# Performance work log

Hardware: AMD Instinct MI355X
Metric: run time of the kernel (lower is better)

Reference implementation:

```python
import jax, jax.numpy as jnp
import numpy as np

UNITS = 1024
OUT_STEPS = 32
NUM_FEATURES = 4
BATCH = 1024
IN_STEPS = 64


def setup_inputs() -> dict:
    key = jax.random.key(0)
    k = jax.random.split(key, 6)
    x = jax.random.normal(k[0], (BATCH, IN_STEPS, NUM_FEATURES), jnp.float32)
    # Keras LSTMCell params: kernel [F,4u], recurrent_kernel [u,4u], bias [4u]
    W = jax.random.normal(k[1], (NUM_FEATURES, 4 * UNITS), jnp.float32) * 0.3
    U = jax.random.normal(k[2], (UNITS, 4 * UNITS), jnp.float32) * 0.03
    b = jnp.zeros((4 * UNITS,), jnp.float32)
    Wd = jax.random.normal(k[3], (UNITS, NUM_FEATURES), jnp.float32) * 0.05
    bd = jnp.zeros((NUM_FEATURES,), jnp.float32)
    return {"x": x, "W": W, "U": U, "b": b, "Wd": Wd, "bd": bd}


def _lstm_cell(xt, h, c, W, U, b):
    # Keras gate order: input, forget, cell, output; sigmoid recurrent act, tanh act
    z = xt @ W + h @ U + b  # [B, 4u]
    i, f, g, o = jnp.split(z, 4, axis=-1)
    c_new = jax.nn.sigmoid(f) * c + jax.nn.sigmoid(i) * jnp.tanh(g)
    h_new = jax.nn.sigmoid(o) * jnp.tanh(c_new)
    return h_new, c_new


def reference(x, W, U, b, Wd, bd):
    B = x.shape[0]
    h0 = jnp.zeros((B, UNITS), x.dtype)
    c0 = jnp.zeros((B, UNITS), x.dtype)

    # warmup: run RNN over the input window, keep final state
    def warm_step(carry, xt):
        h, c = carry
        h, c = _lstm_cell(xt, h, c, W, U, b)
        return (h, c), None

    (h, c), _ = jax.lax.scan(warm_step, (h0, c0), jnp.swapaxes(x, 0, 1))
    pred0 = h @ Wd + bd  # first prediction [B, F]

    def dec_step(carry, _):
        pred, h, c = carry
        h, c = _lstm_cell(pred, h, c, W, U, b)
        pred = h @ Wd + bd
        return (pred, h, c), pred

    _, preds = jax.lax.scan(dec_step, (pred0, h, c), None, length=OUT_STEPS - 1)
    all_preds = jnp.concatenate([pred0[None], preds], axis=0)  # [out_steps, B, F]
    return jnp.transpose(all_preds, (1, 0, 2))  # [B, out_steps, F]
```

## Files before the change

### kernel.cpp

```cpp
#include <hip/hip_runtime.h>

#define BATCH    1024
#define UNITS    1024
#define INSTEPS  64
#define OUTSTEPS 32
#define NF       4
#define NSTEPS   (INSTEPS + OUTSTEPS - 1)

typedef _Float16 half8 __attribute__((ext_vector_type(8)));
typedef float    f32x4 __attribute__((ext_vector_type(4)));

__device__ __forceinline__ float sigf(float x)  { return 1.0f / (1.0f + __expf(-x)); }
__device__ __forceinline__ float tanhf_(float x){ return 1.0f - 2.0f / (__expf(2.0f * x) + 1.0f); }

__global__ void u_transpose(const float* __restrict__ U, _Float16* __restrict__ Ut) {
    __shared__ _Float16 T[64][72];
    const int tid = threadIdx.x;
    const int bid = blockIdx.x;
    const int k0 = (bid >> 6) << 6;
    const int n0 = (bid & 63) << 6;
    #pragma unroll
    for (int i = 0; i < 16; ++i) {
        int q = i * 256 + tid;
        int r = q >> 6, cc = q & 63;
        T[r][cc] = (_Float16)U[(size_t)(k0 + r) * 4096 + n0 + cc];
    }
    __syncthreads();
    #pragma unroll
    for (int i = 0; i < 16; ++i) {
        int q = i * 256 + tid;
        int nn = q >> 6, kk = q & 63;
        Ut[(size_t)(n0 + nn) * 1024 + k0 + kk] = T[kk][nn];
    }
}

#define BS_BYTES  (16*64*64*2)
#define XS_BYTES  (256*4*4)
#define HST_OFF   (BS_BYTES + XS_BYTES)
#define HST_BYTES (256*18*2)
#define LDS_BYTES (HST_OFF + HST_BYTES)

__global__ __launch_bounds__(512, 2) void lstm_seq(
    const float* __restrict__ x, const float* __restrict__ W,
    const float* __restrict__ bias, const float* __restrict__ Wd,
    const float* __restrict__ bd, const _Float16* __restrict__ Ut,
    _Float16* hA, _Float16* hB, float* out, unsigned* bar)
{
    extern __shared__ __align__(16) char smem[];
    _Float16 (*Bs)[64][64] = (_Float16 (*)[64][64])smem;
    float (*xs)[NF] = (float (*)[NF])(smem + BS_BYTES);
    _Float16 (*hst)[18] = (_Float16 (*)[18])(smem + HST_OFF);

    const int tid  = threadIdx.x;
    const int bid  = blockIdx.x;
    const int band = bid & 3;
    const int m0   = band << 8;
    const int u0   = (bid >> 2) << 4;

    const int lane = tid & 63;
    const int wv   = tid >> 6;
    const int quad = lane >> 4;
    const int ln   = lane & 15;

    unsigned* cnt = bar + band * 64;

    const int r_st = tid >> 3;
    const int ck   = tid & 7;
    const int swz  = ((ck ^ (r_st & 7)) << 3);
    const int n_st = ((r_st >> 4) << 10) + u0 + (r_st & 15);
    const _Float16* bsrc = Ut + (size_t)n_st * UNITS + ck * 8;

    #pragma unroll
    for (int kc = 0; kc < 16; ++kc)
        *(float4*)&Bs[kc][r_st][swz] = *(const float4*)(bsrc + kc * 64);

    float wt[4][4], bt[4], btp[4];
    #pragma unroll
    for (int g = 0; g < 4; ++g) {
        int col = (g << 10) + u0 + ln;
        bt[g] = bias[col];
        #pragma unroll
        for (int f = 0; f < 4; ++f) wt[g][f] = W[f * 4096 + col];
    }
    {
        float bdr0 = bd[0], bdr1 = bd[1], bdr2 = bd[2], bdr3 = bd[3];
        #pragma unroll
        for (int g = 0; g < 4; ++g)
            btp[g] = bt[g] + bdr0*wt[g][0] + bdr1*wt[g][1] + bdr2*wt[g][2] + bdr3*wt[g][3];
    }
    const float* wdp = Wd + (size_t)(u0 + ln) * NF;
    float wd0 = wdp[0], wd1 = wdp[1], wd2 = wdp[2], wd3 = wdp[3];
    float bd0 = 0, bd1 = 0, bd2 = 0, bd3 = 0;
    if (u0 == 0) { bd0 = bd[0]; bd1 = bd[1]; bd2 = bd[2]; bd3 = bd[3]; }

    float cr[2][4] = {{0,0,0,0},{0,0,0,0}};
    float hnv[2][4];

    const int swz0 = ((quad ^ (ln & 7)) << 3);
    const int swz1 = swz0 ^ 32;

    const int row0 = m0 + wv * 32 + ln;
    const int aoff = ((quad >> 1) << 15) + row0 * 32 + ((quad & 1) << 4);

    const int xr = tid >> 2, xf = tid & 3;
    float xp0 = x[(size_t)(m0 + xr) * (INSTEPS * NF) + xf];
    float xp1 = x[(size_t)(m0 + 128 + xr) * (INSTEPS * NF) + xf];

    char* const hAc = (char*)hA;
    char* const hBc = (char*)hB;
    const size_t stoff = ((size_t)(u0 >> 4) << 15) + (size_t)(m0 + (tid >> 1)) * 32
                       + ((size_t)(tid & 1) << 4);

    __syncthreads();

    for (int p = 0; p < NSTEPS; ++p) {
        if (p < INSTEPS) {
            xs[xr][xf]       = xp0;
            xs[128 + xr][xf] = xp1;
        } else if (p == INSTEPS) {
            float wc0 = W[n_st], wc1 = W[4096 + n_st],
                  wc2 = W[8192 + n_st], wc3 = W[12288 + n_st];
            #pragma unroll
            for (int kc = 0; kc < 16; ++kc) {
                int k0 = kc * 64 + ck * 8;
                half8 uv = *(const half8*)(bsrc + kc * 64);
                half8 tv;
                #pragma unroll
                for (int j = 0; j < 8; ++j) {
                    const float* wdr = Wd + (size_t)(k0 + j) * NF;
                    float corr = wdr[0]*wc0 + wdr[1]*wc1 + wdr[2]*wc2 + wdr[3]*wc3;
                    tv[j] = (_Float16)((float)uv[j] + corr);
                }
                *(half8*)&Bs[kc][r_st][swz] = tv;
            }
        }
        if (p <= INSTEPS) __syncthreads();

        f32x4 acc[2][4] = {};

        if (p > 0) {
            const char* hb = ((p & 1) ? hAc : hBc) + aoff;
#define AL(kc, j, rr) (*(const half8*)(hb + ((((kc) << 2) + ((j) << 1)) << 15) + ((rr) << 9)))

            half8 ar[6][4];
            #pragma unroll
            for (int d = 0; d < 6; ++d) {
                ar[d][0] = AL(d, 0, 0);
                ar[d][1] = AL(d, 1, 0);
                ar[d][2] = AL(d, 0, 1);
                ar[d][3] = AL(d, 1, 1);
            }

            #pragma unroll
            for (int kc = 0; kc < 16; ++kc) {
                const int sl = kc % 6;
                half8 af0 = ar[sl][0], ag0 = ar[sl][1], af1 = ar[sl][2], ag1 = ar[sl][3];
                if (kc < 10) {
                    ar[sl][0] = AL(kc + 6, 0, 0);
                    ar[sl][1] = AL(kc + 6, 1, 0);
                    ar[sl][2] = AL(kc + 6, 0, 1);
                    ar[sl][3] = AL(kc + 6, 1, 1);
                }
                const _Float16 (*B)[64] = Bs[kc];
                half8 bf0 = *(const half8*)&B[ln][swz0];
                half8 bf1 = *(const half8*)&B[16 + ln][swz0];
                half8 bf2 = *(const half8*)&B[32 + ln][swz0];
                half8 bf3 = *(const half8*)&B[48 + ln][swz0];
                acc[0][0] = __builtin_amdgcn_mfma_f32_16x16x32_f16(af0, bf0, acc[0][0], 0, 0, 0);
                acc[1][0] = __builtin_amdgcn_mfma_f32_16x16x32_f16(af1, bf0, acc[1][0], 0, 0, 0);
                acc[0][1] = __builtin_amdgcn_mfma_f32_16x16x32_f16(af0, bf1, acc[0][1], 0, 0, 0);
                acc[1][1] = __builtin_amdgcn_mfma_f32_16x16x32_f16(af1, bf1, acc[1][1], 0, 0, 0);
                acc[0][2] = __builtin_amdgcn_mfma_f32_16x16x32_f16(af0, bf2, acc[0][2], 0, 0, 0);
                acc[1][2] = __builtin_amdgcn_mfma_f32_16x16x32_f16(af1, bf2, acc[1][2], 0, 0, 0);
                acc[0][3] = __builtin_amdgcn_mfma_f32_16x16x32_f16(af0, bf3, acc[0][3], 0, 0, 0);
                acc[1][3] = __builtin_amdgcn_mfma_f32_16x16x32_f16(af1, bf3, acc[1][3], 0, 0, 0);
                half8 bg0 = *(const half8*)&B[ln][swz1];
                half8 bg1 = *(const half8*)&B[16 + ln][swz1];
                half8 bg2 = *(const half8*)&B[32 + ln][swz1];
                half8 bg3 = *(const half8*)&B[48 + ln][swz1];
                acc[0][0] = __builtin_amdgcn_mfma_f32_16x16x32_f16(ag0, bg0, acc[0][0], 0, 0, 0);
                acc[1][0] = __builtin_amdgcn_mfma_f32_16x16x32_f16(ag1, bg0, acc[1][0], 0, 0, 0);
                acc[0][1] = __builtin_amdgcn_mfma_f32_16x16x32_f16(ag0, bg1, acc[0][1], 0, 0, 0);
                acc[1][1] = __builtin_amdgcn_mfma_f32_16x16x32_f16(ag1, bg1, acc[1][1], 0, 0, 0);
                acc[0][2] = __builtin_amdgcn_mfma_f32_16x16x32_f16(ag0, bg2, acc[0][2], 0, 0, 0);
                acc[1][2] = __builtin_amdgcn_mfma_f32_16x16x32_f16(ag1, bg2, acc[1][2], 0, 0, 0);
                acc[0][3] = __builtin_amdgcn_mfma_f32_16x16x32_f16(ag0, bg3, acc[0][3], 0, 0, 0);
                acc[1][3] = __builtin_amdgcn_mfma_f32_16x16x32_f16(ag1, bg3, acc[1][3], 0, 0, 0);
            }
#undef AL
        }

        const int s_out = p - (INSTEPS - 1);
        #pragma unroll
        for (int r = 0; r < 2; ++r) {
            #pragma unroll
            for (int i = 0; i < 4; ++i) {
                int rl = wv * 32 + r * 16 + quad * 4 + i;
                float zi, zf, zg, zo;
                if (p < INSTEPS) {
                    float x0 = xs[rl][0], x1 = xs[rl][1], x2 = xs[rl][2], x3 = xs[rl][3];
                    zi = acc[r][0][i] + bt[0] + x0*wt[0][0] + x1*wt[0][1] + x2*wt[0][2] + x3*wt[0][3];
                    zf = acc[r][1][i] + bt[1] + x0*wt[1][0] + x1*wt[1][1] + x2*wt[1][2] + x3*wt[1][3];
                    zg = acc[r][2][i] + bt[2] + x0*wt[2][0] + x1*wt[2][1] + x2*wt[2][2] + x3*wt[2][3];
                    zo = acc[r][3][i] + bt[3] + x0*wt[3][0] + x1*wt[3][1] + x2*wt[3][2] + x3*wt[3][3];
                } else {
                    zi = acc[r][0][i] + btp[0];
                    zf = acc[r][1][i] + btp[1];
                    zg = acc[r][2][i] + btp[2];
                    zo = acc[r][3][i] + btp[3];
                }
                float cold = cr[r][i];
                float si = sigf(zi), sf = sigf(zf), so = sigf(zo);
                float cn = sf * cold + si * tanhf_(zg);
                float hn = so * tanhf_(cn);
                cr[r][i] = cn;
                hnv[r][i] = hn;
                hst[rl][ln] = (_Float16)hn;
            }
        }

        const int pn = p + 1;

        {
            char* hw = (p & 1) ? hBc : hAc;
            const unsigned long long* sp = (const unsigned long long*)
                ((const char*)hst + (tid >> 1) * 36 + ((tid & 1) << 4));
            unsigned long long v0 = sp[0], v1 = sp[1];
            unsigned long long* dst = (unsigned long long*)(hw + stoff);
            __hip_atomic_store(dst,     v0, __ATOMIC_RELAXED, __HIP_MEMORY_SCOPE_AGENT);
            __hip_atomic_store(dst + 1, v1, __ATOMIC_RELAXED, __HIP_MEMORY_SCOPE_AGENT);
        }

        __syncthreads();
        if (tid == 0)
            __hip_atomic_fetch_add(cnt, 1u, __ATOMIC_RELAXED, __HIP_MEMORY_SCOPE_AGENT);

        if (s_out >= 0) {
            #pragma unroll
            for (int r = 0; r < 2; ++r) {
                #pragma unroll
                for (int i = 0; i < 4; ++i) {
                    float hn = hnv[r][i];
                    float p0 = hn * wd0, p1 = hn * wd1, p2 = hn * wd2, p3 = hn * wd3;
                    #pragma unroll
                    for (int mk = 1; mk < 16; mk <<= 1) {
                        p0 += __shfl_xor(p0, mk);
                        p1 += __shfl_xor(p1, mk);
                        p2 += __shfl_xor(p2, mk);
                        p3 += __shfl_xor(p3, mk);
                    }
                    if (ln == 0) {
                        int R = m0 + wv * 32 + r * 16 + quad * 4 + i;
                        float* op = out + (size_t)R * (OUTSTEPS * NF) + s_out * NF;
                        atomicAdd(op + 0, p0 + bd0);
                        atomicAdd(op + 1, p1 + bd1);
                        atomicAdd(op + 2, p2 + bd2);
                        atomicAdd(op + 3, p3 + bd3);
                    }
                }
            }
        }

        if (pn < INSTEPS) {
            xp0 = x[(size_t)(m0 + xr) * (INSTEPS * NF) + pn * NF + xf];
            xp1 = x[(size_t)(m0 + 128 + xr) * (INSTEPS * NF) + pn * NF + xf];
        }

        if (tid == 0) {
            const unsigned tgt = (unsigned)pn * 64u;
            while (__hip_atomic_load(cnt, __ATOMIC_RELAXED, __HIP_MEMORY_SCOPE_AGENT) < tgt)
                __builtin_amdgcn_s_sleep(1);
            __builtin_amdgcn_fence(__ATOMIC_ACQUIRE, "agent");
        }
        __syncthreads();
    }
}

extern "C" void kernel_launch(void* const* d_in, const int* in_sizes, int n_in,
                              void* d_out, int out_size, void* d_ws, size_t ws_size,
                              hipStream_t stream) {
    (void)in_sizes; (void)n_in; (void)ws_size;
    const float* x  = (const float*)d_in[0];
    const float* W  = (const float*)d_in[1];
    const float* U  = (const float*)d_in[2];
    const float* b  = (const float*)d_in[3];
    const float* Wd = (const float*)d_in[4];
    const float* bd = (const float*)d_in[5];
    float* out = (float*)d_out;

    char* ws = (char*)d_ws;
    _Float16* hA  = (_Float16*)ws;
    _Float16* hB  = (_Float16*)(ws + (2 << 20));
    _Float16* Ut  = (_Float16*)(ws + (4 << 20));
    unsigned* bar = (unsigned*)(ws + (12 << 20));

    hipMemsetAsync(bar, 0, 4096, stream);
    hipMemsetAsync(d_out, 0, (size_t)out_size * sizeof(float), stream);
    u_transpose<<<1024, 256, 0, stream>>>(U, Ut);

    hipFuncSetAttribute((const void*)lstm_seq,
                        hipFuncAttributeMaxDynamicSharedMemorySize, LDS_BYTES);

    void* args[] = {(void*)&x, (void*)&W, (void*)&b, (void*)&Wd, (void*)&bd,
                    (void*)&Ut, (void*)&hA, (void*)&hB, (void*)&out, (void*)&bar};
    hipLaunchCooperativeKernel((const void*)lstm_seq, dim3(256), dim3(512),
                               args, LDS_BYTES, stream);
}
```

Before: 1.952 ms.

## Replace per-band grid barrier with per-K-chunk group flags consumed inside GEMM

Each band's single counter and full spin barrier at the end of every step are replaced by 16 per-group counters, one per group of 16 blocks. Each counter covers the hidden-state slice that feeds one K-chunk. Before loading a K-chunk of h, a wave waits only on the flag for that chunk's producers and reads h with relaxed agent-scope atomic loads. This lets the recurrent GEMM start on chunks that are already ready, overlapping with blocks that are still finishing. The trade-off is more flag polling per wave, split 8-byte atomic loads in place of 16-byte vector loads, and no acquire fence, which relies on relaxed atomics for visibility. The removed trailing __syncthreads may also leave LDS reuse across steps less protected.

After: 3.453 ms. 1.77x slower.

```diff
diff --git a/kernel.cpp b/kernel.cpp
--- a/kernel.cpp
+++ b/kernel.cpp
@@ -62,7 +62,8 @@
     const int quad = lane >> 4;
     const int ln   = lane & 15;
 
-    unsigned* cnt = bar + band * 64;
+    unsigned* flg = bar + band * 16;
+    const int mygrp = bid >> 4;
 
     const int r_st = tid >> 3;
     const int ck   = tid & 7;
@@ -140,15 +141,42 @@
 
         if (p > 0) {
             const char* hb = ((p & 1) ? hAc : hBc) + aoff;
-#define AL(kc, j, rr) (*(const half8*)(hb + ((((kc) << 2) + ((j) << 1)) << 15) + ((rr) << 9)))
+            const unsigned need = 4u * (unsigned)p;
+
+            unsigned fv = 0xFFFFFFFFu;
+            if (lane < 16)
+                fv = __hip_atomic_load(&flg[lane], __ATOMIC_RELAXED, __HIP_MEMORY_SCOPE_AGENT);
+            unsigned long long rdy = __ballot(fv >= need);
+
+#define WAITG(g) do {                                                           \
+        if (!((rdy >> (g)) & 1)) {                                              \
+            while (__hip_atomic_load(&flg[(g)], __ATOMIC_RELAXED,               \
+                                     __HIP_MEMORY_SCOPE_AGENT) < need)          \
+                __builtin_amdgcn_s_sleep(1);                                    \
+        }                                                                       \
+        asm volatile("" ::: "memory");                                          \
+    } while (0)
+
+#define AL8(dst, off) do {                                                      \
+        unsigned long long _a = __hip_atomic_load(                              \
+            (const unsigned long long*)(hb + (off)),                            \
+            __ATOMIC_RELAXED, __HIP_MEMORY_SCOPE_AGENT);                        \
+        unsigned long long _b = __hip_atomic_load(                              \
+            (const unsigned long long*)(hb + (off) + 8),                        \
+            __ATOMIC_RELAXED, __HIP_MEMORY_SCOPE_AGENT);                        \
+        union { unsigned long long u[2]; half8 h; } _v;                         \
+        _v.u[0] = _a; _v.u[1] = _b; (dst) = _v.h;                               \
+    } while (0)
+#define AOFF(kc, j, rr) (((((kc) << 2) + ((j) << 1)) << 15) + ((rr) << 9))
 
             half8 ar[6][4];
             #pragma unroll
             for (int d = 0; d < 6; ++d) {
-                ar[d][0] = AL(d, 0, 0);
-                ar[d][1] = AL(d, 1, 0);
-                ar[d][2] = AL(d, 0, 1);
-                ar[d][3] = AL(d, 1, 1);
+                WAITG(d);
+                AL8(ar[d][0], AOFF(d, 0, 0));
+                AL8(ar[d][1], AOFF(d, 1, 0));
+                AL8(ar[d][2], AOFF(d, 0, 1));
+                AL8(ar[d][3], AOFF(d, 1, 1));
             }
 
             #pragma unroll
@@ -156,10 +184,11 @@
                 const int sl = kc % 6;
                 half8 af0 = ar[sl][0], ag0 = ar[sl][1], af1 = ar[sl][2], ag1 = ar[sl][3];
                 if (kc < 10) {
-                    ar[sl][0] = AL(kc + 6, 0, 0);
-                    ar[sl][1] = AL(kc + 6, 1, 0);
-                    ar[sl][2] = AL(kc + 6, 0, 1);
-                    ar[sl][3] = AL(kc + 6, 1, 1);
+                    WAITG(kc + 6);
+                    AL8(ar[sl][0], AOFF(kc + 6, 0, 0));
+                    AL8(ar[sl][1], AOFF(kc + 6, 1, 0));
+                    AL8(ar[sl][2], AOFF(kc + 6, 0, 1));
+                    AL8(ar[sl][3], AOFF(kc + 6, 1, 1));
                 }
                 const _Float16 (*B)[64] = Bs[kc];
                 half8 bf0 = *(const half8*)&B[ln][swz0];
@@ -187,7 +216,9 @@
                 acc[0][3] = __builtin_amdgcn_mfma_f32_16x16x32_f16(ag0, bg3, acc[0][3], 0, 0, 0);
                 acc[1][3] = __builtin_amdgcn_mfma_f32_16x16x32_f16(ag1, bg3, acc[1][3], 0, 0, 0);
             }
-#undef AL
+#undef AOFF
+#undef AL8
+#undef WAITG
         }
 
         const int s_out = p - (INSTEPS - 1);
@@ -219,8 +250,6 @@
             }
         }
 
-        const int pn = p + 1;
-
         {
             char* hw = (p & 1) ? hBc : hAc;
             const unsigned long long* sp = (const unsigned long long*)
@@ -233,7 +262,7 @@
 
         __syncthreads();
         if (tid == 0)
-            __hip_atomic_fetch_add(cnt, 1u, __ATOMIC_RELAXED, __HIP_MEMORY_SCOPE_AGENT);
+            __hip_atomic_fetch_add(&flg[mygrp], 1u, __ATOMIC_RELAXED, __HIP_MEMORY_SCOPE_AGENT);
 
         if (s_out >= 0) {
             #pragma unroll
@@ -261,18 +290,11 @@
             }
         }
 
+        const int pn = p + 1;
         if (pn < INSTEPS) {
             xp0 = x[(size_t)(m0 + xr) * (INSTEPS * NF) + pn * NF + xf];
             xp1 = x[(size_t)(m0 + 128 + xr) * (INSTEPS * NF) + pn * NF + xf];
         }
-
-        if (tid == 0) {
-            const unsigned tgt = (unsigned)pn * 64u;
-            while (__hip_atomic_load(cnt, __ATOMIC_RELAXED, __HIP_MEMORY_SCOPE_AGENT) < tgt)
-                __builtin_amdgcn_s_sleep(1);
-            __builtin_amdgcn_fence(__ATOMIC_ACQUIRE, "agent");
-        }
-        __syncthreads();
     }
 }
 
```

## Split K across two wave halves per block with LDS reduction

Applied to the files above, without the earlier changes.

Doubles the block size to 1024 threads and splits the recurrent GEMM's K dimension in half. Each group of 8 waves computes partial sums over 8 k-chunks, and the two halves are combined through an LDS exchange buffer over four rounds of barriers. Only the first half then runs the gate math, the h store and the dense projection. The aim is to shorten the per-step critical path, more waves hiding global h-load latency. The cost is extra LDS traffic, eight more __syncthreads per step, and idle upper waves during the elementwise phase.

After: 1.847 ms. 1.06x faster.

```diff
diff --git a/kernel.cpp b/kernel.cpp
--- a/kernel.cpp
+++ b/kernel.cpp
@@ -38,9 +38,11 @@
 #define XS_BYTES  (256*4*4)
 #define HST_OFF   (BS_BYTES + XS_BYTES)
 #define HST_BYTES (256*18*2)
-#define LDS_BYTES (HST_OFF + HST_BYTES)
-
-__global__ __launch_bounds__(512, 2) void lstm_seq(
+#define XB_OFF    (HST_OFF + HST_BYTES)
+#define XB_BYTES  (2*8*64*16)
+#define LDS_BYTES (XB_OFF + XB_BYTES)
+
+__global__ __launch_bounds__(1024, 4) void lstm_seq(
     const float* __restrict__ x, const float* __restrict__ W,
     const float* __restrict__ bias, const float* __restrict__ Wd,
     const float* __restrict__ bd, const _Float16* __restrict__ Ut,
@@ -50,6 +52,7 @@
     _Float16 (*Bs)[64][64] = (_Float16 (*)[64][64])smem;
     float (*xs)[NF] = (float (*)[NF])(smem + BS_BYTES);
     _Float16 (*hst)[18] = (_Float16 (*)[18])(smem + HST_OFF);
+    f32x4 (*xb)[8][64] = (f32x4 (*)[8][64])(smem + XB_OFF);
 
     const int tid  = threadIdx.x;
     const int bid  = blockIdx.x;
@@ -59,20 +62,24 @@
 
     const int lane = tid & 63;
     const int wv   = tid >> 6;
+    const int rt2  = wv & 7;
+    const int kh   = wv >> 3;
     const int quad = lane >> 4;
     const int ln   = lane & 15;
 
     unsigned* cnt = bar + band * 64;
 
-    const int r_st = tid >> 3;
+    const int r_st = (tid >> 3) & 63;
     const int ck   = tid & 7;
     const int swz  = ((ck ^ (r_st & 7)) << 3);
     const int n_st = ((r_st >> 4) << 10) + u0 + (r_st & 15);
     const _Float16* bsrc = Ut + (size_t)n_st * UNITS + ck * 8;
 
-    #pragma unroll
-    for (int kc = 0; kc < 16; ++kc)
-        *(float4*)&Bs[kc][r_st][swz] = *(const float4*)(bsrc + kc * 64);
+    if (tid < 512) {
+        #pragma unroll
+        for (int kc = 0; kc < 16; ++kc)
+            *(float4*)&Bs[kc][r_st][swz] = *(const float4*)(bsrc + kc * 64);
+    }
 
     float wt[4][4], bt[4], btp[4];
     #pragma unroll
@@ -99,12 +106,11 @@
     const int swz0 = ((quad ^ (ln & 7)) << 3);
     const int swz1 = swz0 ^ 32;
 
-    const int row0 = m0 + wv * 32 + ln;
+    const int row0 = m0 + rt2 * 32 + ln;
     const int aoff = ((quad >> 1) << 15) + row0 * 32 + ((quad & 1) << 4);
 
     const int xr = tid >> 2, xf = tid & 3;
     float xp0 = x[(size_t)(m0 + xr) * (INSTEPS * NF) + xf];
-    float xp1 = x[(size_t)(m0 + 128 + xr) * (INSTEPS * NF) + xf];
 
     char* const hAc = (char*)hA;
     char* const hBc = (char*)hB;
@@ -115,9 +121,8 @@
 
     for (int p = 0; p < NSTEPS; ++p) {
         if (p < INSTEPS) {
-            xs[xr][xf]       = xp0;
-            xs[128 + xr][xf] = xp1;
-        } else if (p == INSTEPS) {
+            xs[xr][xf] = xp0;
+        } else if (p == INSTEPS && tid < 512) {
             float wc0 = W[n_st], wc1 = W[4096 + n_st],
                   wc2 = W[8192 + n_st], wc3 = W[12288 + n_st];
             #pragma unroll
@@ -140,28 +145,30 @@
 
         if (p > 0) {
             const char* hb = ((p & 1) ? hAc : hBc) + aoff;
-#define AL(kc, j, rr) (*(const half8*)(hb + ((((kc) << 2) + ((j) << 1)) << 15) + ((rr) << 9)))
-
-            half8 ar[6][4];
-            #pragma unroll
-            for (int d = 0; d < 6; ++d) {
-                ar[d][0] = AL(d, 0, 0);
-                ar[d][1] = AL(d, 1, 0);
-                ar[d][2] = AL(d, 0, 1);
-                ar[d][3] = AL(d, 1, 1);
-            }
-
-            #pragma unroll
-            for (int kc = 0; kc < 16; ++kc) {
-                const int sl = kc % 6;
+#define AL(kcg, j, rr) (*(const half8*)(hb + ((((kcg) << 2) + ((j) << 1)) << 15) + ((rr) << 9)))
+
+            half8 ar[2][4];
+            #pragma unroll
+            for (int d = 0; d < 2; ++d) {
+                const int kcg = (kh << 3) + d;
+                ar[d][0] = AL(kcg, 0, 0);
+                ar[d][1] = AL(kcg, 1, 0);
+                ar[d][2] = AL(kcg, 0, 1);
+                ar[d][3] = AL(kcg, 1, 1);
+            }
+
+            #pragma unroll
+            for (int kc = 0; kc < 8; ++kc) {
+                const int sl = kc & 1;
                 half8 af0 = ar[sl][0], ag0 = ar[sl][1], af1 = ar[sl][2], ag1 = ar[sl][3];
-                if (kc < 10) {
-                    ar[sl][0] = AL(kc + 6, 0, 0);
-                    ar[sl][1] = AL(kc + 6, 1, 0);
-                    ar[sl][2] = AL(kc + 6, 0, 1);
-                    ar[sl][3] = AL(kc + 6, 1, 1);
-                }
-                const _Float16 (*B)[64] = Bs[kc];
+                if (kc < 6) {
+                    const int kcg = (kh << 3) + kc + 2;
+                    ar[sl][0] = AL(kcg, 0, 0);
+                    ar[sl][1] = AL(kcg, 1, 0);
+                    ar[sl][2] = AL(kcg, 0, 1);
+                    ar[sl][3] = AL(kcg, 1, 1);
+                }
+                const _Float16 (*B)[64] = Bs[(kh << 3) + kc];
                 half8 bf0 = *(const half8*)&B[ln][swz0];
                 half8 bf1 = *(const half8*)&B[16 + ln][swz0];
                 half8 bf2 = *(const half8*)&B[32 + ln][swz0];
@@ -188,54 +195,73 @@
                 acc[1][3] = __builtin_amdgcn_mfma_f32_16x16x32_f16(ag1, bg3, acc[1][3], 0, 0, 0);
             }
 #undef AL
+
+            #pragma unroll
+            for (int r = 0; r < 4; ++r) {
+                if ((wv >> 1) == 4 + r) {
+                    #pragma unroll
+                    for (int j = 0; j < 8; ++j)
+                        xb[wv & 1][j][lane] = acc[j >> 2][j & 3];
+                }
+                __syncthreads();
+                if ((wv >> 1) == r) {
+                    #pragma unroll
+                    for (int j = 0; j < 8; ++j)
+                        acc[j >> 2][j & 3] += xb[wv & 1][j][lane];
+                }
+                __syncthreads();
+            }
         }
 
         const int s_out = p - (INSTEPS - 1);
-        #pragma unroll
-        for (int r = 0; r < 2; ++r) {
-            #pragma unroll
-            for (int i = 0; i < 4; ++i) {
-                int rl = wv * 32 + r * 16 + quad * 4 + i;
-                float zi, zf, zg, zo;
-                if (p < INSTEPS) {
-                    float x0 = xs[rl][0], x1 = xs[rl][1], x2 = xs[rl][2], x3 = xs[rl][3];
-                    zi = acc[r][0][i] + bt[0] + x0*wt[0][0] + x1*wt[0][1] + x2*wt[0][2] + x3*wt[0][3];
-                    zf = acc[r][1][i] + bt[1] + x0*wt[1][0] + x1*wt[1][1] + x2*wt[1][2] + x3*wt[1][3];
-                    zg = acc[r][2][i] + bt[2] + x0*wt[2][0] + x1*wt[2][1] + x2*wt[2][2] + x3*wt[2][3];
-                    zo = acc[r][3][i] + bt[3] + x0*wt[3][0] + x1*wt[3][1] + x2*wt[3][2] + x3*wt[3][3];
-                } else {
-                    zi = acc[r][0][i] + btp[0];
-                    zf = acc[r][1][i] + btp[1];
-                    zg = acc[r][2][i] + btp[2];
-                    zo = acc[r][3][i] + btp[3];
-                }
-                float cold = cr[r][i];
-                float si = sigf(zi), sf = sigf(zf), so = sigf(zo);
-                float cn = sf * cold + si * tanhf_(zg);
-                float hn = so * tanhf_(cn);
-                cr[r][i] = cn;
-                hnv[r][i] = hn;
-                hst[rl][ln] = (_Float16)hn;
+
+        if (kh == 0) {
+            #pragma unroll
+            for (int r = 0; r < 2; ++r) {
+                #pragma unroll
+                for (int i = 0; i < 4; ++i) {
+                    int rl = rt2 * 32 + r * 16 + quad * 4 + i;
+                    float zi, zf, zg, zo;
+                    if (p < INSTEPS) {
+                        float x0 = xs[rl][0], x1 = xs[rl][1], x2 = xs[rl][2], x3 = xs[rl][3];
+                        zi = acc[r][0][i] + bt[0] + x0*wt[0][0] + x1*wt[0][1] + x2*wt[0][2] + x3*wt[0][3];
+                        zf = acc[r][1][i] + bt[1] + x0*wt[1][0] + x1*wt[1][1] + x2*wt[1][2] + x3*wt[1][3];
+                        zg = acc[r][2][i] + bt[2] + x0*wt[2][0] + x1*wt[2][1] + x2*wt[2][2] + x3*wt[2][3];
+                        zo = acc[r][3][i] + bt[3] + x0*wt[3][0] + x1*wt[3][1] + x2*wt[3][2] + x3*wt[3][3];
+                    } else {
+                        zi = acc[r][0][i] + btp[0];
+                        zf = acc[r][1][i] + btp[1];
+                        zg = acc[r][2][i] + btp[2];
+                        zo = acc[r][3][i] + btp[3];
+                    }
+                    float cold = cr[r][i];
+                    float si = sigf(zi), sf = sigf(zf), so = sigf(zo);
+                    float cn = sf * cold + si * tanhf_(zg);
+                    float hn = so * tanhf_(cn);
+                    cr[r][i] = cn;
+                    hnv[r][i] = hn;
+                    hst[rl][ln] = (_Float16)hn;
+                }
+            }
+
+            {
+                char* hw = (p & 1) ? hBc : hAc;
+                const unsigned long long* sp = (const unsigned long long*)
+                    ((const char*)hst + (tid >> 1) * 36 + ((tid & 1) << 4));
+                unsigned long long v0 = sp[0], v1 = sp[1];
+                unsigned long long* dst = (unsigned long long*)(hw + stoff);
+                __hip_atomic_store(dst,     v0, __ATOMIC_RELAXED, __HIP_MEMORY_SCOPE_AGENT);
+                __hip_atomic_store(dst + 1, v1, __ATOMIC_RELAXED, __HIP_MEMORY_SCOPE_AGENT);
             }
         }
 
         const int pn = p + 1;
-
-        {
-            char* hw = (p & 1) ? hBc : hAc;
-            const unsigned long long* sp = (const unsigned long long*)
-                ((const char*)hst + (tid >> 1) * 36 + ((tid & 1) << 4));
-            unsigned long long v0 = sp[0], v1 = sp[1];
-            unsigned long long* dst = (unsigned long long*)(hw + stoff);
-            __hip_atomic_store(dst,     v0, __ATOMIC_RELAXED, __HIP_MEMORY_SCOPE_AGENT);
-            __hip_atomic_store(dst + 1, v1, __ATOMIC_RELAXED, __HIP_MEMORY_SCOPE_AGENT);
-        }
 
         __syncthreads();
         if (tid == 0)
             __hip_atomic_fetch_add(cnt, 1u, __ATOMIC_RELAXED, __HIP_MEMORY_SCOPE_AGENT);
 
-        if (s_out >= 0) {
+        if (kh == 0 && s_out >= 0) {
             #pragma unroll
             for (int r = 0; r < 2; ++r) {
                 #pragma unroll
@@ -250,7 +276,7 @@
                         p3 += __shfl_xor(p3, mk);
                     }
                     if (ln == 0) {
-                        int R = m0 + wv * 32 + r * 16 + quad * 4 + i;
+                        int R = m0 + rt2 * 32 + r * 16 + quad * 4 + i;
                         float* op = out + (size_t)R * (OUTSTEPS * NF) + s_out * NF;
                         atomicAdd(op + 0, p0 + bd0);
                         atomicAdd(op + 1, p1 + bd1);
@@ -263,7 +289,6 @@
 
         if (pn < INSTEPS) {
             xp0 = x[(size_t)(m0 + xr) * (INSTEPS * NF) + pn * NF + xf];
-            xp1 = x[(size_t)(m0 + 128 + xr) * (INSTEPS * NF) + pn * NF + xf];
         }
 
         if (tid == 0) {
@@ -303,6 +328,6 @@
 
     void* args[] = {(void*)&x, (void*)&W, (void*)&b, (void*)&Wd, (void*)&bd,
                     (void*)&Ut, (void*)&hA, (void*)&hB, (void*)&out, (void*)&bar};
-    hipLaunchCooperativeKernel((const void*)lstm_seq, dim3(256), dim3(512),
+    hipLaunchCooperativeKernel((const void*)lstm_seq, dim3(256), dim3(1024),
                                args, LDS_BYTES, stream);
 }
```
